# Optimization experiments

Measured on AMD Instinct MI355X. Metric: run time of the kernel, lower is better.

The kernel has to match this reference:

```python
import jax, jax.numpy as jnp
import numpy as np
from math import sqrt


def setup_inputs() -> dict:
    key = jax.random.key(0)
    ks = jax.random.split(key, 5)
    B, S, D = 4, 2048, 1024
    scale = 0.02
    return {
        "x": jax.random.normal(ks[0], (B, S, D), dtype=jnp.float32),
        "Wq": jax.random.normal(ks[1], (D, D), dtype=jnp.float32) * scale,
        "Wk": jax.random.normal(ks[2], (D, D), dtype=jnp.float32) * scale,
        "Wv": jax.random.normal(ks[3], (D, D), dtype=jnp.float32) * scale,
        "Wo": jax.random.normal(ks[4], (D, D), dtype=jnp.float32) * scale,
    }


def reference(x, Wq, Wk, Wv, Wo):
    NUM_HEAD = 16
    B, S, D = x.shape
    d_k = D // NUM_HEAD

    # fused QKV projection: weights are (d_model, d_in), applied as W @ x^T -> x @ W^T
    q = jnp.einsum('od,bsd->bso', Wq, x)
    k = jnp.einsum('od,bsd->bso', Wk, x)
    v = jnp.einsum('od,bsd->bso', Wv, x)

    def split_heads(t):  # [B,S,D] -> [B,H,S,d_k]
        return t.reshape(B, S, NUM_HEAD, d_k).transpose(0, 2, 1, 3)

    q, k, v = split_heads(q), split_heads(k), split_heads(v)

    # naive causal attention: full [B,H,S,S] score matrix
    scores = jnp.einsum('bhqd,bhkd->bhqk', q, k) / sqrt(d_k)
    causal = jnp.tril(jnp.ones((S, S), dtype=bool))  # [S,S]
    scores = jnp.where(causal, scores, -jnp.inf)
    probs = jax.nn.softmax(scores, axis=-1)
    attn = jnp.einsum('bhqk,bhkd->bhqd', probs, v)

    # merge heads: [B,H,S,d_k] -> [B,S,D]
    attn = attn.transpose(0, 2, 1, 3).reshape(B, S, D)
    # output projection
    return jnp.einsum('om,bsm->bso', Wo, attn)
```

## Files before the change

kernel.cpp:

```cpp
#include <hip/hip_runtime.h>
#include <hip/hip_bf16.h>
#include <stdint.h>

typedef unsigned short u16;
typedef __attribute__((ext_vector_type(8))) short bf16x8;
typedef __attribute__((ext_vector_type(4))) float f32x4;
typedef __attribute__((ext_vector_type(16))) float f32x16;

#define AS1 __attribute__((address_space(1)))
#define AS3 __attribute__((address_space(3)))

__device__ __forceinline__ u16 f2bf(float f) {
  union { float f; uint32_t u; } v; v.f = f;
  uint32_t u = v.u;
  return (u16)((u + 0x7FFFu + ((u >> 16) & 1u)) >> 16);
}

__device__ __forceinline__ uint32_t cvtpk(float lo, float hi) {
  uint32_t d;
  asm("v_cvt_pk_bf16_f32 %0, %1, %2" : "=v"(d) : "v"(lo), "v"(hi));
  return d;
}

__global__ __launch_bounds__(256) void cvt_all_kernel(const float* __restrict__ x,
    const float* __restrict__ Wq, const float* __restrict__ Wk,
    const float* __restrict__ Wv, const float* __restrict__ Wo,
    u16* __restrict__ xb, u16* __restrict__ wqb, u16* __restrict__ wkb,
    u16* __restrict__ wvb, u16* __restrict__ wob) {
  const int bid = blockIdx.x;
  const float* s;
  u16* d;
  int i;
  if (bid < 8192) {
    s = x; d = xb; i = bid * 256 + threadIdx.x;
  } else {
    const int w = (bid - 8192) >> 10;
    i = ((bid - 8192) & 1023) * 256 + threadIdx.x;
    s = (w == 0) ? Wq : (w == 1) ? Wk : (w == 2) ? Wv : Wo;
    d = (w == 0) ? wqb : (w == 1) ? wkb : (w == 2) ? wvb : wob;
  }
  float4 v = reinterpret_cast<const float4*>(s)[i];
  uint2 o;
  o.x = cvtpk(v.x, v.y);
  o.y = cvtpk(v.z, v.w);
  reinterpret_cast<uint2*>(d)[i] = o;
}

#define QSCALE 0.18033688011112042f

#define GK 64

template <int MODE, int KC, typename OutT>
__device__ __forceinline__ void gemm128_body(u16* __restrict__ lds,
    const u16* __restrict__ A, const u16* __restrict__ Bm, OutT* __restrict__ C,
    int M, int N, int by, int bx, float oscale) {
  const int tid = threadIdx.x;
  const int lane = tid & 63;
  const int wave = tid >> 6;
  const int wm = wave >> 1, wn = wave & 1;
  const int l15 = lane & 15, lhi = lane >> 4;
  const int axor = (lane & 7) << 4;

  const int srow = tid >> 3;
  const int scol = (((tid & 7) ^ (srow & 7)) << 4);
  const size_t Kb = (size_t)KC * 2;
  const uint8_t* Ag = (const uint8_t*)A + (size_t)(by * 128 + srow) * Kb + scol;
  const uint8_t* Bg = (const uint8_t*)Bm + (size_t)(bx * 128 + srow) * Kb + scol;
  uint8_t* Lb = (uint8_t*)lds;

#define STG128(bufi, kt)                                                                  \
  do {                                                                                    \
    _Pragma("unroll") for (int c = 0; c < 4; ++c) {                                       \
      __builtin_amdgcn_global_load_lds(                                                   \
          (const AS1 uint32_t*)(Ag + (size_t)c * 32 * Kb + (size_t)(kt) * 128),           \
          (AS3 uint32_t*)(Lb + (bufi) * 32768 + c * 4096 + tid * 16), 16, 0, 0);          \
      __builtin_amdgcn_global_load_lds(                                                   \
          (const AS1 uint32_t*)(Bg + (size_t)c * 32 * Kb + (size_t)(kt) * 128),           \
          (AS3 uint32_t*)(Lb + (bufi) * 32768 + 16384 + c * 4096 + tid * 16), 16, 0, 0);  \
    }                                                                                     \
  } while (0)

  const f32x4 fzero = {0.f, 0.f, 0.f, 0.f};
  f32x4 acc[4][4];
#pragma unroll
  for (int m = 0; m < 4; ++m)
#pragma unroll
    for (int n = 0; n < 4; ++n) acc[m][n] = fzero;

  constexpr int NT = KC / GK;

  STG128(0, 0);
  __syncthreads();

#pragma unroll
  for (int t = 0; t < NT; ++t) {
    const int cur = t & 1;
    if (t + 1 < NT) STG128(cur ^ 1, t + 1);
    const uint8_t* Ab = Lb + cur * 32768;
    const uint8_t* Bb = Ab + 16384;
    bf16x8 aF[4][2], bF[4][2];
#pragma unroll
    for (int ff = 0; ff < 4; ++ff)
#pragma unroll
      for (int ks = 0; ks < 2; ++ks) {
        aF[ff][ks] = *reinterpret_cast<const bf16x8*>(
            Ab + (wm * 64 + ff * 16 + l15) * 128 + ((ks * 64 + lhi * 16) ^ axor));
        bF[ff][ks] = *reinterpret_cast<const bf16x8*>(
            Bb + (wn * 64 + ff * 16 + l15) * 128 + ((ks * 64 + lhi * 16) ^ axor));
      }
    __builtin_amdgcn_s_setprio(1);
#pragma unroll
    for (int mm = 0; mm < 4; ++mm)
#pragma unroll
      for (int nn = 0; nn < 4; ++nn)
#pragma unroll
        for (int ks = 0; ks < 2; ++ks)
          acc[mm][nn] = __builtin_amdgcn_mfma_f32_16x16x32_bf16(aF[mm][ks], bF[nn][ks],
                                                                acc[mm][nn], 0, 0, 0);
    __builtin_amdgcn_s_setprio(0);
    __syncthreads();
  }

#pragma unroll
  for (int mf = 0; mf < 4; ++mf)
#pragma unroll
    for (int nf = 0; nf < 4; ++nf) {
      const int row0 = by * 128 + wm * 64 + mf * 16 + lhi * 4;
      const int col = bx * 128 + wn * 64 + nf * 16 + l15;
      if constexpr (MODE == 2) {
        uint2 pk;
        pk.x = cvtpk(acc[mf][nf][0], acc[mf][nf][1]);
        pk.y = cvtpk(acc[mf][nf][2], acc[mf][nf][3]);
        *reinterpret_cast<uint2*>((u16*)C + (size_t)col * M + row0) = pk;
      } else if constexpr (MODE == 1) {
#pragma unroll
        for (int r = 0; r < 4; ++r)
          ((float*)C)[(size_t)(row0 + r) * N + col] = acc[mf][nf][r];
      } else {
#pragma unroll
        for (int r = 0; r < 4; ++r)
          ((u16*)C)[(size_t)(row0 + r) * N + col] = f2bf(acc[mf][nf][r] * oscale);
      }
    }
#undef STG128
}

__global__ __launch_bounds__(256, 2) void gemm_qkv_kernel(const u16* __restrict__ A,
    const u16* __restrict__ W0, const u16* __restrict__ W1, const u16* __restrict__ W2,
    u16* __restrict__ OQ, u16* __restrict__ OK, u16* __restrict__ OVT, int M, int N) {
  __shared__ u16 lds[2][2][128 * GK];
  const int id = blockIdx.x;
  const int xcd = id & 7;
  const int slot = id >> 3;
  const int bz = slot >> 6;
  const int r = slot & 63;
  const int byi = r >> 3, bx = r & 7;
  const int by = xcd + 8 * byi;
  if (bz == 0)      gemm128_body<0, 1024, u16>(&lds[0][0][0], A, W0, OQ,  M, N, by, bx, QSCALE);
  else if (bz == 1) gemm128_body<0, 1024, u16>(&lds[0][0][0], A, W1, OK,  M, N, by, bx, 1.f);
  else              gemm128_body<2, 1024, u16>(&lds[0][0][0], A, W2, OVT, M, N, by, bx, 1.f);
}

__global__ __launch_bounds__(256, 2) void gemm_out_kernel(const u16* __restrict__ A,
    const u16* __restrict__ Bm, float* __restrict__ C, int M, int N) {
  __shared__ u16 lds[2][2][128 * GK];
  const int id = blockIdx.x;
  const int xcd = id & 7;
  const int slot = id >> 3;
  const int byi = slot >> 3, bx = slot & 7;
  const int by = xcd + 8 * byi;
  gemm128_body<1, 1024, float>(&lds[0][0][0], A, Bm, C, M, N, by, bx, 1.f);
}

#define KVB 128

__device__ __forceinline__ void attn_bb(const u16* __restrict__ KB,
    const u16* __restrict__ VB, const bf16x8 (&qf)[4], f32x16 (&acc)[2],
    float& mrow, float& lrow, int kvb, int qr, bool boundary, int bb, int l31, int lh) {
  f32x16 sc;
#pragma unroll
  for (int r = 0; r < 16; ++r) sc[r] = 0.f;
#pragma unroll
  for (int dc = 0; dc < 4; ++dc) {
    const bf16x8 kf = *reinterpret_cast<const bf16x8*>(
        KB + (bb * 32 + l31) * 64 + (((dc * 2 + lh) ^ (l31 & 7)) << 3));
    sc = __builtin_amdgcn_mfma_f32_32x32x16_bf16(kf, qf[dc], sc, 0, 0, 0);
  }
  if (boundary) {
#pragma unroll
    for (int r = 0; r < 16; ++r) {
      const int kvg = kvb + (r & 3) + 8 * (r >> 2) + 4 * lh;
      sc[r] = (kvg > qr) ? -1e30f : sc[r];
    }
  }
  float t0 = fmaxf(sc[0], sc[8]),  t1 = fmaxf(sc[1], sc[9]);
  float t2 = fmaxf(sc[2], sc[10]), t3 = fmaxf(sc[3], sc[11]);
  float t4 = fmaxf(sc[4], sc[12]), t5 = fmaxf(sc[5], sc[13]);
  float t6 = fmaxf(sc[6], sc[14]), t7 = fmaxf(sc[7], sc[15]);
  t0 = fmaxf(t0, t4); t1 = fmaxf(t1, t5); t2 = fmaxf(t2, t6); t3 = fmaxf(t3, t7);
  float bmax = fmaxf(fmaxf(t0, t1), fmaxf(t2, t3));
  bmax = fmaxf(bmax, __shfl_xor(bmax, 32, 64));
  if (!__all(bmax <= mrow + 6.f)) {
    const float mn = fmaxf(mrow, bmax);
    const float fac = __builtin_amdgcn_exp2f(mrow - mn);
    mrow = mn;
    lrow *= fac;
    acc[0] *= fac;
    acc[1] *= fac;
  }
#pragma unroll
  for (int r = 0; r < 16; ++r) sc[r] = __builtin_amdgcn_exp2f(sc[r] - mrow);
  float s0 = sc[0] + sc[8],  s1 = sc[1] + sc[9];
  float s2 = sc[2] + sc[10], s3 = sc[3] + sc[11];
  float s4 = sc[4] + sc[12], s5 = sc[5] + sc[13];
  float s6 = sc[6] + sc[14], s7 = sc[7] + sc[15];
  s0 += s4; s1 += s5; s2 += s6; s3 += s7;
  lrow += (s0 + s1) + (s2 + s3);
#pragma unroll
  for (int cc = 0; cc < 2; ++cc) {
    uint32_t a0 = cvtpk(sc[8 * cc + 0], sc[8 * cc + 1]);
    uint32_t a1 = cvtpk(sc[8 * cc + 2], sc[8 * cc + 3]);
    uint32_t b0 = cvtpk(sc[8 * cc + 4], sc[8 * cc + 5]);
    uint32_t b1 = cvtpk(sc[8 * cc + 6], sc[8 * cc + 7]);
    asm("v_permlane32_swap_b32 %0, %1" : "+v"(a0), "+v"(b0));
    asm("v_permlane32_swap_b32 %0, %1" : "+v"(a1), "+v"(b1));
    union { uint32_t u[4]; bf16x8 v8; } pf;
    pf.u[0] = a0; pf.u[1] = a1; pf.u[2] = b0; pf.u[3] = b1;
    const int c2 = bb * 2 + cc;
#pragma unroll
    for (int db = 0; db < 2; ++db) {
      const int blkv = ((c2 * 2 + lh) & 8) | (((c2 * 2 + lh) ^ (l31 & 7)) & 7);
      const bf16x8 vfg = *reinterpret_cast<const bf16x8*>(
          VB + (db * 32 + l31) * 128 + blkv * 8);
      acc[db] = __builtin_amdgcn_mfma_f32_32x32x16_bf16(vfg, pf.v8, acc[db], 0, 0, 0);
    }
  }
}

__global__ __launch_bounds__(256, 2) void attn_kernel(const u16* __restrict__ Q,
    const u16* __restrict__ Kg, const u16* __restrict__ VTg, u16* __restrict__ O,
    int S, int H, int Dm, int T) {
  const int bh = blockIdx.x;
  const int b = bh / H, h = bh % H;
  const int y = blockIdx.y;
  const int qh0 = 1920 - 128 * y;
  const int ql0 = 128 * y;
  const int tid = threadIdx.x;
  const int lane = tid & 63, wave = tid >> 6;
  const int l31 = lane & 31, lh = lane >> 5;

  __shared__ u16 KVs[2][2][8192];

  const u16* Qh = Q + ((size_t)b * S) * Dm + h * 64;
  const u16* Kh = Kg + ((size_t)b * S) * Dm + h * 64;
  const u16* Vh = VTg + (size_t)(h * 64) * T + (size_t)b * S;
  const int qvH = qh0 + wave * 32, qvL = ql0 + wave * 32;
  const int qrH = qvH + l31, qrL = qvL + l31;

  bf16x8 qfH[4], qfL[4];
#pragma unroll
  for (int dc = 0; dc < 4; ++dc) {
    qfH[dc] = *reinterpret_cast<const bf16x8*>(Qh + (size_t)qrH * Dm + dc * 16 + lh * 8);
    qfL[dc] = *reinterpret_cast<const bf16x8*>(Qh + (size_t)qrL * Dm + dc * 16 + lh * 8);
  }

  f32x16 accH[2], accL[2];
#pragma unroll
  for (int db = 0; db < 2; ++db)
#pragma unroll
    for (int r = 0; r < 16; ++r) { accH[db][r] = 0.f; accL[db][r] = 0.f; }
  float mH = -1e30f, lH = 0.f, mL = -1e30f, lL = 0.f;

#define STAGE(bufi, kvoff)                                                                     \
  do {                                                                                         \
    const int rK = tid >> 3;                                                                   \
    const int cK = (((tid & 7) ^ (rK & 7)) << 3);                                              \
    const int rV = tid >> 4;                                                                   \
    const int sV = tid & 15;                                                                   \
    const int cV = (((sV & 8) | ((sV ^ (rV & 7)) & 7)) << 3);                                  \
    _Pragma("unroll") for (int j = 0; j < 4; ++j) {                                            \
      __builtin_amdgcn_global_load_lds(                                                        \
          (const AS1 uint32_t*)(Kh + (size_t)((kvoff) + j * 32 + rK) * Dm + cK),               \
          (AS3 uint32_t*)(&KVs[bufi][0][j * 2048 + tid * 8]), 16, 0, 0);                       \
      __builtin_amdgcn_global_load_lds(                                                        \
          (const AS1 uint32_t*)(Vh + (size_t)(j * 16 + rV) * T + (kvoff) + cV),                \
          (AS3 uint32_t*)(&KVs[bufi][1][j * 2048 + tid * 8]), 16, 0, 0);                       \
    }                                                                                          \
  } while (0)

  const int nt = 16 - y;
  STAGE(0, 0);
  int buf = 0;

  for (int t = 0; t < nt; ++t) {
    __syncthreads();
    const int kv = t * KVB;
    if (t + 1 < nt) STAGE(buf ^ 1, (t + 1) * KVB);
    const u16* KB = KVs[buf][0];
    const u16* VB = KVs[buf][1];
#pragma unroll
    for (int bb = 0; bb < 4; ++bb) {
      const int kvb = kv + bb * 32;
      if (kvb <= qvH + 31)
        attn_bb(KB, VB, qfH, accH, mH, lH, kvb, qrH, (kvb + 31 > qvH), bb, l31, lh);
    }
#pragma unroll
    for (int bb = 0; bb < 4; ++bb) {
      const int kvb = kv + bb * 32;
      if (kvb <= qvL + 31)
        attn_bb(KB, VB, qfL, accL, mL, lL, kvb, qrL, (kvb + 31 > qvL), bb, l31, lh);
    }
    buf ^= 1;
  }

  lH += __shfl_xor(lH, 32, 64);
  lL += __shfl_xor(lL, 32, 64);
  const float invH = 1.f / lH, invL = 1.f / lL;
  __syncthreads();
  u16* Ost = &KVs[0][0][0];
  {
#pragma unroll
    for (int s = 0; s < 2; ++s) {
      const int row = s * 128 + wave * 32 + l31;
      const f32x16* ac = s ? accL : accH;
      const float inv = s ? invL : invH;
#pragma unroll
      for (int db = 0; db < 2; ++db)
#pragma unroll
        for (int g = 0; g < 4; ++g) {
          uint2 pk;
          pk.x = cvtpk(ac[db][4 * g + 0] * inv, ac[db][4 * g + 1] * inv);
          pk.y = cvtpk(ac[db][4 * g + 2] * inv, ac[db][4 * g + 3] * inv);
          const int blk = 4 * db + g;
          const int addr = row * 64 + (((blk ^ (row & 7)) << 3)) + 4 * lh;
          *reinterpret_cast<uint2*>(Ost + addr) = pk;
        }
    }
  }
  __syncthreads();
#pragma unroll
  for (int p = 0; p < 8; ++p) {
    const int idx = p * 256 + tid;
    const int row = idx >> 3, seg = idx & 7;
    const float4 v = *reinterpret_cast<const float4*>(Ost + row * 64 + ((seg ^ (row & 7)) << 3));
    const int q = (row < 128) ? (qh0 + row) : (ql0 + row - 128);
    *reinterpret_cast<float4*>(O + ((size_t)b * S + q) * Dm + h * 64 + seg * 8) = v;
  }
#undef STAGE
}

extern "C" void kernel_launch(void* const* d_in, const int* in_sizes, int n_in,
                              void* d_out, int out_size, void* d_ws, size_t ws_size,
                              hipStream_t stream) {
  const float* x  = (const float*)d_in[0];
  const float* Wq = (const float*)d_in[1];
  const float* Wk = (const float*)d_in[2];
  const float* Wv = (const float*)d_in[3];
  const float* Wo = (const float*)d_in[4];
  float* out = (float*)d_out;

  const int B = 4, S = 2048, D = 1024, H = 16;
  const int T = B * S;

  uint8_t* p = (uint8_t*)d_ws;
  u16* xb  = (u16*)p; p += (size_t)T * D * 2;
  u16* wqb = (u16*)p; p += (size_t)D * D * 2;
  u16* wkb = (u16*)p; p += (size_t)D * D * 2;
  u16* wvb = (u16*)p; p += (size_t)D * D * 2;
  u16* wob = (u16*)p; p += (size_t)D * D * 2;
  u16* Qb  = (u16*)p; p += (size_t)T * D * 2;
  u16* Kb  = (u16*)p; p += (size_t)T * D * 2;
  u16* VTb = (u16*)p; p += (size_t)D * T * 2;
  u16* Ab  = xb;

  cvt_all_kernel<<<dim3(12288), dim3(256), 0, stream>>>(x, Wq, Wk, Wv, Wo,
                                                        xb, wqb, wkb, wvb, wob);

  gemm_qkv_kernel<<<dim3(1536), dim3(256), 0, stream>>>(xb, wqb, wkb, wvb, Qb, Kb, VTb, T, D);

  attn_kernel<<<dim3(B * H, 8), dim3(256), 0, stream>>>(Qb, Kb, VTb, Ab, S, H, D, T);

  gemm_out_kernel<<<dim3(512), dim3(256), 0, stream>>>(Ab, wob, out, T, D);
}
```

Before: 136.7 us.

## Split attention KV range across two wave groups with in-block softmax merge

The attention block grows to 512 threads as two groups of four waves. Each group processes alternating 64-key halves of every 128-key stage, and the groups merge their partial online-softmax states (max, sum, accumulators) through LDS at the end. This halves the serial KV loop length per wave and raises wave-level parallelism per block. The cost is a larger LDS footprint, an extra merge phase with additional barriers, and higher per-CU register demand that may limit occupancy.

```diff
diff --git a/kernel.cpp b/kernel.cpp
--- a/kernel.cpp
+++ b/kernel.cpp
@@ -172,7 +172,7 @@
   gemm128_body<1, 1024, float>(&lds[0][0][0], A, Bm, C, M, N, by, bx, 1.f);
 }
 
-#define KVB 128
+#define KVB 64
 
 __device__ __forceinline__ void attn_bb(const u16* __restrict__ KB,
     const u16* __restrict__ VB, const bf16x8 (&qf)[4], f32x16 (&acc)[2],
@@ -229,15 +229,14 @@
     const int c2 = bb * 2 + cc;
 #pragma unroll
     for (int db = 0; db < 2; ++db) {
-      const int blkv = ((c2 * 2 + lh) & 8) | (((c2 * 2 + lh) ^ (l31 & 7)) & 7);
       const bf16x8 vfg = *reinterpret_cast<const bf16x8*>(
-          VB + (db * 32 + l31) * 128 + blkv * 8);
+          VB + (db * 32 + l31) * 64 + (((c2 * 2 + lh) ^ (l31 & 7)) << 3));
       acc[db] = __builtin_amdgcn_mfma_f32_32x32x16_bf16(vfg, pf.v8, acc[db], 0, 0, 0);
     }
   }
 }
 
-__global__ __launch_bounds__(256, 2) void attn_kernel(const u16* __restrict__ Q,
+__global__ __launch_bounds__(512, 4) void attn_kernel(const u16* __restrict__ Q,
     const u16* __restrict__ Kg, const u16* __restrict__ VTg, u16* __restrict__ O,
     int S, int H, int Dm, int T) {
   const int bh = blockIdx.x;
@@ -247,14 +246,17 @@
   const int ql0 = 128 * y;
   const int tid = threadIdx.x;
   const int lane = tid & 63, wave = tid >> 6;
+  const int wg = wave >> 2;
+  const int w4 = wave & 3;
   const int l31 = lane & 31, lh = lane >> 5;
 
-  __shared__ u16 KVs[2][2][8192];
+  __shared__ __align__(16) uint8_t SMEM[73728];
+  u16* SK = (u16*)SMEM;
 
   const u16* Qh = Q + ((size_t)b * S) * Dm + h * 64;
   const u16* Kh = Kg + ((size_t)b * S) * Dm + h * 64;
   const u16* Vh = VTg + (size_t)(h * 64) * T + (size_t)b * S;
-  const int qvH = qh0 + wave * 32, qvL = ql0 + wave * 32;
+  const int qvH = qh0 + w4 * 32, qvL = ql0 + w4 * 32;
   const int qrH = qvH + l31, qrL = qvL + l31;
 
   bf16x8 qfH[4], qfL[4];
@@ -271,41 +273,40 @@
     for (int r = 0; r < 16; ++r) { accH[db][r] = 0.f; accL[db][r] = 0.f; }
   float mH = -1e30f, lH = 0.f, mL = -1e30f, lL = 0.f;
 
-#define STAGE(bufi, kvoff)                                                                     \
+  const int srow = tid >> 3;
+  const int scolb = (((tid & 7) ^ (srow & 7)) << 3);
+
+#define STAGE_PAIR(bufi, si_)                                                                  \
   do {                                                                                         \
-    const int rK = tid >> 3;                                                                   \
-    const int cK = (((tid & 7) ^ (rK & 7)) << 3);                                              \
-    const int rV = tid >> 4;                                                                   \
-    const int sV = tid & 15;                                                                   \
-    const int cV = (((sV & 8) | ((sV ^ (rV & 7)) & 7)) << 3);                                  \
-    _Pragma("unroll") for (int j = 0; j < 4; ++j) {                                            \
+    const int kv0 = (si_) * 128;                                                               \
+    _Pragma("unroll") for (int g = 0; g < 2; ++g) {                                            \
       __builtin_amdgcn_global_load_lds(                                                        \
-          (const AS1 uint32_t*)(Kh + (size_t)((kvoff) + j * 32 + rK) * Dm + cK),               \
-          (AS3 uint32_t*)(&KVs[bufi][0][j * 2048 + tid * 8]), 16, 0, 0);                       \
+          (const AS1 uint32_t*)(Kh + (size_t)(kv0 + g * 64 + srow) * Dm + scolb),              \
+          (AS3 uint32_t*)(SK + (bufi) * 16384 + g * 8192 + tid * 8), 16, 0, 0);                \
       __builtin_amdgcn_global_load_lds(                                                        \
-          (const AS1 uint32_t*)(Vh + (size_t)(j * 16 + rV) * T + (kvoff) + cV),                \
-          (AS3 uint32_t*)(&KVs[bufi][1][j * 2048 + tid * 8]), 16, 0, 0);                       \
+          (const AS1 uint32_t*)(Vh + (size_t)srow * T + kv0 + g * 64 + scolb),                 \
+          (AS3 uint32_t*)(SK + (bufi) * 16384 + g * 8192 + 4096 + tid * 8), 16, 0, 0);         \
     }                                                                                          \
   } while (0)
 
-  const int nt = 16 - y;
-  STAGE(0, 0);
+  const int nsi = 16 - y;
+  STAGE_PAIR(0, 0);
   int buf = 0;
 
-  for (int t = 0; t < nt; ++t) {
+  for (int si = 0; si < nsi; ++si) {
     __syncthreads();
-    const int kv = t * KVB;
-    if (t + 1 < nt) STAGE(buf ^ 1, (t + 1) * KVB);
-    const u16* KB = KVs[buf][0];
-    const u16* VB = KVs[buf][1];
-#pragma unroll
-    for (int bb = 0; bb < 4; ++bb) {
+    if (si + 1 < nsi) STAGE_PAIR(buf ^ 1, si + 1);
+    const u16* KB = SK + buf * 16384 + wg * 8192;
+    const u16* VB = KB + 4096;
+    const int kv = (2 * si + wg) * KVB;
+#pragma unroll
+    for (int bb = 0; bb < 2; ++bb) {
       const int kvb = kv + bb * 32;
       if (kvb <= qvH + 31)
         attn_bb(KB, VB, qfH, accH, mH, lH, kvb, qrH, (kvb + 31 > qvH), bb, l31, lh);
     }
 #pragma unroll
-    for (int bb = 0; bb < 4; ++bb) {
+    for (int bb = 0; bb < 2; ++bb) {
       const int kvb = kv + bb * 32;
       if (kvb <= qvL + 31)
         attn_bb(KB, VB, qfL, accL, mL, lL, kvb, qrL, (kvb + 31 > qvL), bb, l31, lh);
@@ -315,13 +316,58 @@
 
   lH += __shfl_xor(lH, 32, 64);
   lL += __shfl_xor(lL, 32, 64);
-  const float invH = 1.f / lH, invL = 1.f / lL;
+
+  float* MG = (float*)SMEM;
+  const int mi = (w4 * 64 + lane) * 72;
   __syncthreads();
-  u16* Ost = &KVs[0][0][0];
-  {
+  if (wg == 1) {
+#pragma unroll
+    for (int db = 0; db < 2; ++db)
+#pragma unroll
+      for (int r = 0; r < 16; ++r) {
+        MG[mi + db * 16 + r] = accH[db][r];
+        MG[mi + 32 + db * 16 + r] = accL[db][r];
+      }
+    MG[mi + 64] = mH; MG[mi + 65] = lH;
+    MG[mi + 66] = mL; MG[mi + 67] = lL;
+  }
+  __syncthreads();
+  float invH = 0.f, invL = 0.f;
+  if (wg == 0) {
+    const float mBH = MG[mi + 64], lBH = MG[mi + 65];
+    const float mBL = MG[mi + 66], lBL = MG[mi + 67];
+    {
+      const float mm = fmaxf(mH, mBH);
+      const float fa = __builtin_amdgcn_exp2f(mH - mm);
+      const float fb = __builtin_amdgcn_exp2f(mBH - mm);
+      lH = lH * fa + lBH * fb;
+#pragma unroll
+      for (int db = 0; db < 2; ++db)
+#pragma unroll
+        for (int r = 0; r < 16; ++r)
+          accH[db][r] = accH[db][r] * fa + MG[mi + db * 16 + r] * fb;
+    }
+    {
+      const float mm = fmaxf(mL, mBL);
+      const float fa = __builtin_amdgcn_exp2f(mL - mm);
+      const float fb = __builtin_amdgcn_exp2f(mBL - mm);
+      lL = lL * fa + lBL * fb;
+#pragma unroll
+      for (int db = 0; db < 2; ++db)
+#pragma unroll
+        for (int r = 0; r < 16; ++r)
+          accL[db][r] = accL[db][r] * fa + MG[mi + 32 + db * 16 + r] * fb;
+    }
+    invH = 1.f / lH;
+    invL = 1.f / lL;
+  }
+  __syncthreads();
+
+  u16* Ost = (u16*)SMEM;
+  if (wg == 0) {
 #pragma unroll
     for (int s = 0; s < 2; ++s) {
-      const int row = s * 128 + wave * 32 + l31;
+      const int row = s * 128 + w4 * 32 + l31;
       const f32x16* ac = s ? accL : accH;
       const float inv = s ? invL : invH;
 #pragma unroll
@@ -339,14 +385,14 @@
   }
   __syncthreads();
 #pragma unroll
-  for (int p = 0; p < 8; ++p) {
-    const int idx = p * 256 + tid;
+  for (int p = 0; p < 4; ++p) {
+    const int idx = p * 512 + tid;
     const int row = idx >> 3, seg = idx & 7;
     const float4 v = *reinterpret_cast<const float4*>(Ost + row * 64 + ((seg ^ (row & 7)) << 3));
     const int q = (row < 128) ? (qh0 + row) : (ql0 + row - 128);
     *reinterpret_cast<float4*>(O + ((size_t)b * S + q) * Dm + h * 64 + seg * 8) = v;
   }
-#undef STAGE
+#undef STAGE_PAIR
 }
 
 extern "C" void kernel_launch(void* const* d_in, const int* in_sizes, int n_in,
@@ -378,7 +424,7 @@
 
   gemm_qkv_kernel<<<dim3(1536), dim3(256), 0, stream>>>(xb, wqb, wkb, wvb, Qb, Kb, VTb, T, D);
 
-  attn_kernel<<<dim3(B * H, 8), dim3(256), 0, stream>>>(Qb, Kb, VTb, Ab, S, H, D, T);
+  attn_kernel<<<dim3(B * H, 8), dim3(512), 0, stream>>>(Qb, Kb, VTb, Ab, S, H, D, T);
 
   gemm_out_kernel<<<dim3(512), dim3(256), 0, stream>>>(Ab, wob, out, T, D);
 }
```

After: 170.9 us. 1.25x slower.

## Split attention into one query tile per block with smaller KV tiles

Applied to the files above, without the earlier changes.

Replaces the paired high/low query-tile scheme, where each block handled two 128-row query tiles to balance causal work, with one 128-row query tile per block. The grid doubles to 16 in y, launched heaviest tiles first. KV staging tiles shrink from 128 to 64 rows, which halves LDS use and allows four blocks per CU instead of two. The aim is higher occupancy and more blocks to hide latency, at the cost of losing the built-in load balancing and doubling the number of barrier/stage iterations per unit of work.

```diff
diff --git a/kernel.cpp b/kernel.cpp
--- a/kernel.cpp
+++ b/kernel.cpp
@@ -172,7 +172,7 @@
   gemm128_body<1, 1024, float>(&lds[0][0][0], A, Bm, C, M, N, by, bx, 1.f);
 }
 
-#define KVB 128
+#define KVB 64
 
 __device__ __forceinline__ void attn_bb(const u16* __restrict__ KB,
     const u16* __restrict__ VB, const bf16x8 (&qf)[4], f32x16 (&acc)[2],
@@ -229,66 +229,59 @@
     const int c2 = bb * 2 + cc;
 #pragma unroll
     for (int db = 0; db < 2; ++db) {
-      const int blkv = ((c2 * 2 + lh) & 8) | (((c2 * 2 + lh) ^ (l31 & 7)) & 7);
       const bf16x8 vfg = *reinterpret_cast<const bf16x8*>(
-          VB + (db * 32 + l31) * 128 + blkv * 8);
+          VB + (db * 32 + l31) * 64 + (((c2 * 2 + lh) ^ (l31 & 7)) << 3));
       acc[db] = __builtin_amdgcn_mfma_f32_32x32x16_bf16(vfg, pf.v8, acc[db], 0, 0, 0);
     }
   }
 }
 
-__global__ __launch_bounds__(256, 2) void attn_kernel(const u16* __restrict__ Q,
+__global__ __launch_bounds__(256, 4) void attn_kernel(const u16* __restrict__ Q,
     const u16* __restrict__ Kg, const u16* __restrict__ VTg, u16* __restrict__ O,
     int S, int H, int Dm, int T) {
   const int bh = blockIdx.x;
   const int b = bh / H, h = bh % H;
-  const int y = blockIdx.y;
-  const int qh0 = 1920 - 128 * y;
-  const int ql0 = 128 * y;
+  const int s = 15 - blockIdx.y;
+  const int q0 = 128 * s;
   const int tid = threadIdx.x;
   const int lane = tid & 63, wave = tid >> 6;
   const int l31 = lane & 31, lh = lane >> 5;
 
-  __shared__ u16 KVs[2][2][8192];
+  __shared__ u16 KVs[2][2][64 * 64];
 
   const u16* Qh = Q + ((size_t)b * S) * Dm + h * 64;
   const u16* Kh = Kg + ((size_t)b * S) * Dm + h * 64;
   const u16* Vh = VTg + (size_t)(h * 64) * T + (size_t)b * S;
-  const int qvH = qh0 + wave * 32, qvL = ql0 + wave * 32;
-  const int qrH = qvH + l31, qrL = qvL + l31;
-
-  bf16x8 qfH[4], qfL[4];
-#pragma unroll
-  for (int dc = 0; dc < 4; ++dc) {
-    qfH[dc] = *reinterpret_cast<const bf16x8*>(Qh + (size_t)qrH * Dm + dc * 16 + lh * 8);
-    qfL[dc] = *reinterpret_cast<const bf16x8*>(Qh + (size_t)qrL * Dm + dc * 16 + lh * 8);
-  }
-
-  f32x16 accH[2], accL[2];
+  const int qv = q0 + wave * 32;
+  const int qr = qv + l31;
+
+  bf16x8 qf[4];
+#pragma unroll
+  for (int dc = 0; dc < 4; ++dc)
+    qf[dc] = *reinterpret_cast<const bf16x8*>(Qh + (size_t)qr * Dm + dc * 16 + lh * 8);
+
+  f32x16 acc[2];
 #pragma unroll
   for (int db = 0; db < 2; ++db)
 #pragma unroll
-    for (int r = 0; r < 16; ++r) { accH[db][r] = 0.f; accL[db][r] = 0.f; }
-  float mH = -1e30f, lH = 0.f, mL = -1e30f, lL = 0.f;
+    for (int r = 0; r < 16; ++r) acc[db][r] = 0.f;
+  float mrow = -1e30f, lrow = 0.f;
 
 #define STAGE(bufi, kvoff)                                                                     \
   do {                                                                                         \
-    const int rK = tid >> 3;                                                                   \
-    const int cK = (((tid & 7) ^ (rK & 7)) << 3);                                              \
-    const int rV = tid >> 4;                                                                   \
-    const int sV = tid & 15;                                                                   \
-    const int cV = (((sV & 8) | ((sV ^ (rV & 7)) & 7)) << 3);                                  \
-    _Pragma("unroll") for (int j = 0; j < 4; ++j) {                                            \
+    const int sr = tid >> 3;                                                                   \
+    const int sc_ = (((tid & 7) ^ (sr & 7)) << 3);                                             \
+    _Pragma("unroll") for (int j = 0; j < 2; ++j) {                                            \
       __builtin_amdgcn_global_load_lds(                                                        \
-          (const AS1 uint32_t*)(Kh + (size_t)((kvoff) + j * 32 + rK) * Dm + cK),               \
+          (const AS1 uint32_t*)(Kh + (size_t)((kvoff) + j * 32 + sr) * Dm + sc_),              \
           (AS3 uint32_t*)(&KVs[bufi][0][j * 2048 + tid * 8]), 16, 0, 0);                       \
       __builtin_amdgcn_global_load_lds(                                                        \
-          (const AS1 uint32_t*)(Vh + (size_t)(j * 16 + rV) * T + (kvoff) + cV),                \
+          (const AS1 uint32_t*)(Vh + (size_t)(j * 32 + sr) * T + (kvoff) + sc_),               \
           (AS3 uint32_t*)(&KVs[bufi][1][j * 2048 + tid * 8]), 16, 0, 0);                       \
     }                                                                                          \
   } while (0)
 
-  const int nt = 16 - y;
+  const int nt = 2 * s + 2;
   STAGE(0, 0);
   int buf = 0;
 
@@ -299,52 +292,39 @@
     const u16* KB = KVs[buf][0];
     const u16* VB = KVs[buf][1];
 #pragma unroll
-    for (int bb = 0; bb < 4; ++bb) {
+    for (int bb = 0; bb < 2; ++bb) {
       const int kvb = kv + bb * 32;
-      if (kvb <= qvH + 31)
-        attn_bb(KB, VB, qfH, accH, mH, lH, kvb, qrH, (kvb + 31 > qvH), bb, l31, lh);
-    }
-#pragma unroll
-    for (int bb = 0; bb < 4; ++bb) {
-      const int kvb = kv + bb * 32;
-      if (kvb <= qvL + 31)
-        attn_bb(KB, VB, qfL, accL, mL, lL, kvb, qrL, (kvb + 31 > qvL), bb, l31, lh);
+      if (kvb <= qv + 31)
+        attn_bb(KB, VB, qf, acc, mrow, lrow, kvb, qr, (kvb + 31 > qv), bb, l31, lh);
     }
     buf ^= 1;
   }
 
-  lH += __shfl_xor(lH, 32, 64);
-  lL += __shfl_xor(lL, 32, 64);
-  const float invH = 1.f / lH, invL = 1.f / lL;
+  lrow += __shfl_xor(lrow, 32, 64);
+  const float inv = 1.f / lrow;
   __syncthreads();
   u16* Ost = &KVs[0][0][0];
   {
-#pragma unroll
-    for (int s = 0; s < 2; ++s) {
-      const int row = s * 128 + wave * 32 + l31;
-      const f32x16* ac = s ? accL : accH;
-      const float inv = s ? invL : invH;
-#pragma unroll
-      for (int db = 0; db < 2; ++db)
-#pragma unroll
-        for (int g = 0; g < 4; ++g) {
-          uint2 pk;
-          pk.x = cvtpk(ac[db][4 * g + 0] * inv, ac[db][4 * g + 1] * inv);
-          pk.y = cvtpk(ac[db][4 * g + 2] * inv, ac[db][4 * g + 3] * inv);
-          const int blk = 4 * db + g;
-          const int addr = row * 64 + (((blk ^ (row & 7)) << 3)) + 4 * lh;
-          *reinterpret_cast<uint2*>(Ost + addr) = pk;
-        }
-    }
+    const int row = wave * 32 + l31;
+#pragma unroll
+    for (int db = 0; db < 2; ++db)
+#pragma unroll
+      for (int g = 0; g < 4; ++g) {
+        uint2 pk;
+        pk.x = cvtpk(acc[db][4 * g + 0] * inv, acc[db][4 * g + 1] * inv);
+        pk.y = cvtpk(acc[db][4 * g + 2] * inv, acc[db][4 * g + 3] * inv);
+        const int blk = 4 * db + g;
+        const int addr = row * 64 + (((blk ^ (row & 7)) << 3)) + 4 * lh;
+        *reinterpret_cast<uint2*>(Ost + addr) = pk;
+      }
   }
   __syncthreads();
 #pragma unroll
-  for (int p = 0; p < 8; ++p) {
+  for (int p = 0; p < 4; ++p) {
     const int idx = p * 256 + tid;
     const int row = idx >> 3, seg = idx & 7;
     const float4 v = *reinterpret_cast<const float4*>(Ost + row * 64 + ((seg ^ (row & 7)) << 3));
-    const int q = (row < 128) ? (qh0 + row) : (ql0 + row - 128);
-    *reinterpret_cast<float4*>(O + ((size_t)b * S + q) * Dm + h * 64 + seg * 8) = v;
+    *reinterpret_cast<float4*>(O + ((size_t)b * S + q0 + row) * Dm + h * 64 + seg * 8) = v;
   }
 #undef STAGE
 }
@@ -378,7 +358,7 @@
 
   gemm_qkv_kernel<<<dim3(1536), dim3(256), 0, stream>>>(xb, wqb, wkb, wvb, Qb, Kb, VTb, T, D);
 
-  attn_kernel<<<dim3(B * H, 8), dim3(256), 0, stream>>>(Qb, Kb, VTb, Ab, S, H, D, T);
+  attn_kernel<<<dim3(B * H, 16), dim3(256), 0, stream>>>(Qb, Kb, VTb, Ab, S, H, D, T);
 
   gemm_out_kernel<<<dim3(512), dim3(256), 0, stream>>>(Ab, wob, out, T, D);
 }
```

New measurement: 133.7 us. -2.2%, faster.
